# Performance work log

Hardware: AMD Instinct MI355X
Metric: run time of the kernel (lower is better)

## Reference

```python
import jax, jax.numpy as jnp
import numpy as np

KS = 3          # deformable kernel size
PAD = 1         # zero padding
N = KS * KS     # sampling points per pixel
INC = 64
OUTC = 64


def _conv(x, w, stride, pad, groups):
    return jax.lax.conv_general_dilated(
        x, w, (stride, stride), ((pad, pad), (pad, pad)),
        feature_group_count=groups,
        dimension_numbers=('NCHW', 'OIHW', 'NCHW'))


def setup_inputs() -> dict:
    key = jax.random.key(0)
    k = jax.random.split(key, 5)
    b, h, w = 4, 128, 128
    x = jax.random.normal(k[0], (b, INC, h, w), jnp.float32)
    # SeparableConv2d params (bias=False throughout in source)
    p_dw = jax.random.normal(k[1], (INC, 1, 3, 3), jnp.float32) * 0.1     # p_conv depthwise 3x3 pad1
    p_pw = jax.random.normal(k[2], (2 * N, INC, 1, 1), jnp.float32) * 0.1  # p_conv pointwise -> 2N offsets
    c_dw = jax.random.normal(k[3], (INC, 1, KS, KS), jnp.float32) * 0.1    # conv depthwise k=ks stride=ks
    c_pw = jax.random.normal(k[4], (OUTC, INC, 1, 1), jnp.float32) * 0.1   # conv pointwise
    return {'x': x, 'p_dw': p_dw, 'p_pw': p_pw, 'c_dw': c_dw, 'c_pw': c_pw}


def reference(x, p_dw, p_pw, c_dw, c_pw):
    b, c, h, w = x.shape
    offset = _conv(_conv(x, p_dw, 1, 1, INC), p_pw, 1, 0, 1)   # [b, 2N, h, w]
    xp = jnp.pad(x, ((0, 0), (0, 0), (PAD, PAD), (PAD, PAD)))  # zero_padding
    Hp, Wp = h + 2 * PAD, w + 2 * PAD
    # p_n: kernel-relative offsets (row-major over ks x ks, 'ij' meshgrid)
    r = jnp.arange(-(KS - 1) // 2, (KS - 1) // 2 + 1, dtype=jnp.float32)
    pnx, pny = jnp.meshgrid(r, r, indexing='ij')
    p_n = jnp.concatenate([pnx.ravel(), pny.ravel()])[None, :, None, None]  # [1, 2N, 1, 1]
    # p_0: base grid, 1-indexed (accounts for padding), stride=1
    gx = jnp.arange(1, h + 1, dtype=jnp.float32)[None, None, :, None]
    gy = jnp.arange(1, w + 1, dtype=jnp.float32)[None, None, None, :]
    p0 = jnp.concatenate([jnp.broadcast_to(gx, (1, N, h, w)),
                          jnp.broadcast_to(gy, (1, N, h, w))], axis=1)      # [1, 2N, h, w]
    p = (p0 + p_n + offset).transpose(0, 2, 3, 1)                           # [b, h, w, 2N]
    px, py = p[..., :N], p[..., N:]
    fx, fy = jnp.floor(px), jnp.floor(py)
    ltx = jnp.clip(fx, 0, Hp - 1); lty = jnp.clip(fy, 0, Wp - 1)
    rbx = jnp.clip(fx + 1, 0, Hp - 1); rby = jnp.clip(fy + 1, 0, Wp - 1)
    pxc = jnp.clip(px, 0, Hp - 1); pyc = jnp.clip(py, 0, Wp - 1)
    # bilinear weights
    g_lt = (1 + (ltx - pxc)) * (1 + (lty - pyc))
    g_rb = (1 - (rbx - pxc)) * (1 - (rby - pyc))
    g_lb = (1 + (ltx - pxc)) * (1 - (rby - pyc))
    g_rt = (1 - (rbx - pxc)) * (1 + (lty - pyc))
    x_flat = xp.reshape(b, c, Hp * Wp)

    def gather(qx, qy):  # -> [b, c, h, w, N]
        idx = (qx * Wp + qy).astype(jnp.int32).reshape(b, 1, h * w * N)
        return jnp.take_along_axis(x_flat, idx, axis=2).reshape(b, c, h, w, N)

    x_off = (g_lt[:, None] * gather(ltx, lty) + g_rb[:, None] * gather(rbx, rby)
             + g_lb[:, None] * gather(ltx, rby) + g_rt[:, None] * gather(rbx, lty))
    # _reshape_x_offset: [b,c,h,w,N] -> [b,c,h*ks,w*ks]
    x_off = x_off.reshape(b, c, h, w, KS, KS).transpose(0, 1, 2, 4, 3, 5).reshape(b, c, h * KS, w * KS)
    # SeparableConv2d(inc, outc, k=ks, stride=ks)
    return _conv(_conv(x_off, c_dw, KS, 0, INC), c_pw, 1, 0, 1)
```

## Files before the change

### kernel.cpp

```cpp
#include <hip/hip_runtime.h>
#include <hip/hip_fp16.h>

#define Hdim 128
#define Wdim 128
#define Cdim 64
#define HW   (Hdim * Wdim)
#define NPIX (4 * HW)
#define NBLK (NPIX / 64)
#define NXCD 8
#define Hp 130
#define HWp (Hp * Hp)

typedef _Float16 v8h __attribute__((ext_vector_type(8)));
typedef float    v4f __attribute__((ext_vector_type(4)));

__device__ __forceinline__ int xcd_swizzle(int bid, int nblk) {
    return (bid % NXCD) * (nblk / NXCD) + bid / NXCD;
}

__global__ __launch_bounds__(512) void transpose_kernel(
    const float* __restrict__ x,
    __half* __restrict__ xt)
{
    __shared__ float tile[64][65];
    int lane = threadIdx.x & 63;
    int g    = threadIdx.x >> 6;
    int blk  = xcd_swizzle(blockIdx.x, NBLK);
    int pix0 = blk * 64;
    int b    = pix0 >> 14;
    int hw0  = pix0 & (HW - 1);
    int h    = hw0 >> 7;
    int w0   = hw0 & 127;

    {
        int gid = blockIdx.x * 512 + threadIdx.x;
        if (gid < 2064 * 8) {
            int rp  = gid >> 3, sub = gid & 7;
            int img = rp / 516, pos = rp - img * 516;
            int i, j;
            if (pos < 130)      { i = 0;   j = pos; }
            else if (pos < 260) { i = 129; j = pos - 130; }
            else { int p2 = pos - 260; i = 1 + (p2 >> 1); j = (p2 & 1) ? 129 : 0; }
            float4* dst = (float4*)(xt + ((size_t)img * HWp + i * Hp + j) * Cdim);
            dst[sub] = make_float4(0.f, 0.f, 0.f, 0.f);
        }
    }

#pragma unroll
    for (int i = 0; i < 8; ++i) {
        int c = g * 8 + i;
        tile[c][lane] = x[(size_t)(b * Cdim + c) * HW + hw0 + lane];
    }
    __syncthreads();
#pragma unroll
    for (int i = 0; i < 8; ++i) {
        int p = g * 8 + i;
        size_t ppos = ((size_t)b * HWp + (h + 1) * Hp + (w0 + 1 + p)) * Cdim + lane;
        xt[ppos] = (__half)tile[lane][p];
    }
}

__global__ __launch_bounds__(512) void fused_kernel(
    const float* __restrict__ x,
    const float* __restrict__ p_dw,
    const float* __restrict__ p_pw,
    const __half* __restrict__ xt,
    const float* __restrict__ c_dw,
    const float* __restrict__ c_pw,
    float* __restrict__ out)
{
    __shared__ __align__(16) unsigned char smem[26880];
    __shared__ __align__(16) unsigned int geoL[8][320];

    auto part_h = (_Float16 (*)[18][64])smem;
    auto accs_h = (_Float16 (*)[72])smem;
    auto outD   = (float (*)[69])(smem + 9216);

    int lane = threadIdx.x & 63;
    int g    = threadIdx.x >> 6;
    int blk  = xcd_swizzle(blockIdx.x, NBLK);
    int pix0 = blk * 64;
    int pix  = pix0 + lane;
    int w = pix & (Wdim - 1);
    int h = (pix >> 7) & (Hdim - 1);
    int b = pix >> 14;

    int   off9[9];
    float msk9[9];
#pragma unroll
    for (int dh = -1; dh <= 1; ++dh) {
#pragma unroll
        for (int dw = -1; dw <= 1; ++dw) {
            int tap = (dh + 1) * 3 + (dw + 1);
            int hh = h + dh, ww = w + dw;
            bool ok = (hh >= 0) & (hh < Hdim) & (ww >= 0) & (ww < Wdim);
            off9[tap] = ok ? hh * Wdim + ww : 0;
            msk9[tap] = ok ? 1.f : 0.f;
        }
    }

    float t[8];
#pragma unroll
    for (int i = 0; i < 8; ++i) {
        int c = g * 8 + i;
        const float* xb0 = x + (size_t)(b * Cdim + c) * HW;
        float s = 0.f;
#pragma unroll
        for (int tap = 0; tap < 9; ++tap) {
            float v = xb0[off9[tap]] * msk9[tap];
            s += v * p_dw[c * 9 + tap];
        }
        t[i] = s;
    }

#pragma unroll
    for (int j = 0; j < 18; ++j) {
        float s = 0.f;
#pragma unroll
        for (int i = 0; i < 8; ++i)
            s += p_pw[j * Cdim + g * 8 + i] * t[i];
        part_h[g][j][lane] = (_Float16)s;
    }
    __syncthreads();

#pragma unroll
    for (int it = 0; it < 2; ++it) {
        int idx = threadIdx.x + it * 512;
        if (idx < 9 * 64) {
            int k = idx >> 6;
            int p = idx & 63;

            float offx = 0.f, offy = 0.f;
#pragma unroll
            for (int q = 0; q < 8; ++q) {
                offx += (float)part_h[q][k][p];
                offy += (float)part_h[q][k + 9][p];
            }

            int ppix = pix0 + p;
            int pw2 = ppix & (Wdim - 1);
            int ph2 = (ppix >> 7) & (Hdim - 1);

            float px = (float)(ph2 + 1) + (float)(k / 3 - 1) + offx;
            float py = (float)(pw2 + 1) + (float)(k % 3 - 1) + offy;

            float fx = floorf(px), fy = floorf(py);
            float ltx = fminf(fmaxf(fx, 0.f), 129.f);
            float lty = fminf(fmaxf(fy, 0.f), 129.f);
            float rbx = fminf(fmaxf(fx + 1.f, 0.f), 129.f);
            float rby = fminf(fmaxf(fy + 1.f, 0.f), 129.f);
            float pxc = fminf(fmaxf(px, 0.f), 129.f);
            float pyc = fminf(fmaxf(py, 0.f), 129.f);

            float glt = (1.f + ltx - pxc) * (1.f + lty - pyc);
            float grb = (1.f - rbx + pxc) * (1.f - rby + pyc);
            float glb = (1.f + ltx - pxc) * (1.f - rby + pyc);
            float grt = (1.f - rbx + pxc) * (1.f + lty - pyc);

            int ix0 = (int)ltx, iy0 = (int)lty, ix1 = (int)rbx, iy1 = (int)rby;

            unsigned int bb1, bb2;
            if (iy1 == iy0 + 1) {
                bb1 = (unsigned int)(ix0 * Hp + iy0) << 7;
                bb2 = (unsigned int)(ix1 * Hp + iy0) << 7;
            } else {
                glt = glb = grt = grb = 0.f;
                bb1 = bb2 = 0;
            }

            __half2 wlo = __floats2half2_rn(glt, grt);
            __half2 whi = __floats2half2_rn(glb, grb);
            uint4 pk;
            pk.x = *(const unsigned int*)&wlo;
            pk.y = *(const unsigned int*)&whi;
            pk.z = bb1;
            pk.w = bb2;
            *(uint4*)&geoL[p >> 3][(k * 8 + (p & 7)) * 4] = pk;
        }
    }
    __syncthreads();

    int c2   = lane & 31;
    bool lo  = lane < 32;
    int gu   = __builtin_amdgcn_readfirstlane(g);
    const char* xbB = (const char*)(xt + (size_t)b * HWp * Cdim) + (lane << 2);

    int gv0, gv1, gv2, gv3, gv4;
    {
        const unsigned int* gb = &geoL[gu][0] + lane;
        gv0 = gb[0];   gv1 = gb[64];  gv2 = gb[128];
        gv3 = gb[192]; gv4 = gb[256];
    }
    __half2 wk2h[9];
#pragma unroll
    for (int k = 0; k < 9; ++k)
        wk2h[k] = __floats2half2_rn(c_dw[(2 * c2) * 9 + k],
                                    c_dw[(2 * c2 + 1) * 9 + k]);

#define GV(r) ((r)==0?gv0:(r)==1?gv1:(r)==2?gv2:(r)==3?gv3:gv4)
#define RL(f) __builtin_amdgcn_readlane(GV((f) >> 6), (f) & 63)

    __half2 acch[8];
#pragma unroll
    for (int i = 0; i < 8; ++i) acch[i] = __floats2half2_rn(0.f, 0.f);

#pragma unroll
    for (int k = 0; k < 9; ++k) {
#pragma unroll
        for (int i = 0; i < 8; ++i) {
            const int f = (k * 8 + i) * 4;
            unsigned int d0 = (unsigned int)RL(f + 0);
            unsigned int d1 = (unsigned int)RL(f + 1);
            unsigned int bb1 = (unsigned int)RL(f + 2);
            unsigned int bb2 = (unsigned int)RL(f + 3);
            unsigned int v1 = *(const unsigned int*)(xbB + bb1);
            unsigned int v2 = *(const unsigned int*)(xbB + bb2);
            unsigned int wsu = lo ? d0 : d1;
            __half2 w12 = *(const __half2*)&wsu;
            __half2 v1h = *(const __half2*)&v1;
            __half2 v2h = *(const __half2*)&v2;
            __half2 tt = __hfma2(v2h, __half2half2(__high2half(w12)),
                                 __hmul2(v1h, __half2half2(__low2half(w12))));
            acch[i] = __hfma2(wk2h[k], tt, acch[i]);
        }
    }
#undef RL
#undef GV

#pragma unroll
    for (int i = 0; i < 8; ++i) {
        int me = *(int*)&acch[i];
        int ot = __shfl_xor(me, 32);
        acch[i] = __hadd2(acch[i], *(__half2*)&ot);
    }
    if (lo) {
#pragma unroll
        for (int i = 0; i < 8; ++i)
            *(__half2*)&accs_h[gu * 8 + i][2 * c2] = acch[i];
    }
    __syncthreads();

    {
        int pb = gu & 3;
        int ob = gu >> 2;
        int lr = lane & 15;
        int lg = lane >> 4;

        const v8h a0 = *(const v8h*)&accs_h[pb * 16 + lr][lg * 8];
        const v8h a1 = *(const v8h*)&accs_h[pb * 16 + lr][32 + lg * 8];

        v4f d0 = {0.f, 0.f, 0.f, 0.f}, d1 = {0.f, 0.f, 0.f, 0.f};
#pragma unroll
        for (int t2 = 0; t2 < 2; ++t2) {
            int oc = ob * 32 + t2 * 16 + lr;
            const float* wr = c_pw + oc * Cdim + lg * 8;
            v8h b0, b1;
#pragma unroll
            for (int j = 0; j < 8; ++j) {
                b0[j] = (_Float16)wr[j];
                b1[j] = (_Float16)wr[32 + j];
            }
            if (t2 == 0) {
                d0 = __builtin_amdgcn_mfma_f32_16x16x32_f16(a0, b0, d0, 0, 0, 0);
                d0 = __builtin_amdgcn_mfma_f32_16x16x32_f16(a1, b1, d0, 0, 0, 0);
            } else {
                d1 = __builtin_amdgcn_mfma_f32_16x16x32_f16(a0, b0, d1, 0, 0, 0);
                d1 = __builtin_amdgcn_mfma_f32_16x16x32_f16(a1, b1, d1, 0, 0, 0);
            }
        }

#pragma unroll
        for (int r = 0; r < 4; ++r) {
            outD[pb * 16 + lg * 4 + r][ob * 32 + lr]      = d0[r];
            outD[pb * 16 + lg * 4 + r][ob * 32 + 16 + lr] = d1[r];
        }
    }
    __syncthreads();

    int hw = pix & (HW - 1);
    size_t obase = (size_t)b * Cdim * HW + hw;
#pragma unroll
    for (int i = 0; i < 8; ++i)
        out[obase + (size_t)(gu * 8 + i) * HW] = outD[lane][gu * 8 + i];
}

extern "C" void kernel_launch(void* const* d_in, const int* in_sizes, int n_in,
                              void* d_out, int out_size, void* d_ws, size_t ws_size,
                              hipStream_t stream) {
    const float* x    = (const float*)d_in[0];
    const float* p_dw = (const float*)d_in[1];
    const float* p_pw = (const float*)d_in[2];
    const float* c_dw = (const float*)d_in[3];
    const float* c_pw = (const float*)d_in[4];
    float* out = (float*)d_out;

    __half* xt = (__half*)d_ws;

    transpose_kernel<<<dim3(NBLK), dim3(512), 0, stream>>>(x, xt);
    fused_kernel<<<dim3(NBLK), dim3(512), 0, stream>>>(x, p_dw, p_pw, xt, c_dw, c_pw, out);
}
```

Baseline: 50.88 us.

## Restructure deformable gather to 16-byte loads with lane-split corners and shuffle reduction

```diff
diff --git a/kernel.cpp b/kernel.cpp
--- a/kernel.cpp
+++ b/kernel.cpp
@@ -71,13 +71,15 @@
 {
     __shared__ __align__(16) unsigned char smem[26880];
     __shared__ __align__(16) unsigned int geoL[8][320];
+    __shared__ __align__(16) _Float16 cdw_h[9][64];
 
     auto part_h = (_Float16 (*)[18][64])smem;
     auto accs_h = (_Float16 (*)[72])smem;
     auto outD   = (float (*)[69])(smem + 9216);
 
-    int lane = threadIdx.x & 63;
-    int g    = threadIdx.x >> 6;
+    int tid  = threadIdx.x;
+    int lane = tid & 63;
+    int g    = tid >> 6;
     int blk  = xcd_swizzle(blockIdx.x, NBLK);
     int pix0 = blk * 64;
     int pix  = pix0 + lane;
@@ -121,11 +123,15 @@
             s += p_pw[j * Cdim + g * 8 + i] * t[i];
         part_h[g][j][lane] = (_Float16)s;
     }
+    for (int idx = tid; idx < 9 * 64; idx += 512) {
+        int k = idx >> 6, ch = idx & 63;
+        cdw_h[k][ch] = (_Float16)c_dw[ch * 9 + k];
+    }
     __syncthreads();
 
 #pragma unroll
     for (int it = 0; it < 2; ++it) {
-        int idx = threadIdx.x + it * 512;
+        int idx = tid + it * 512;
         if (idx < 9 * 64) {
             int k = idx >> 6;
             int p = idx & 63;
@@ -168,75 +174,81 @@
                 bb1 = bb2 = 0;
             }
 
-            __half2 wlo = __floats2half2_rn(glt, grt);
-            __half2 whi = __floats2half2_rn(glb, grb);
+            __half2 wr0 = __floats2half2_rn(glt, glb);
+            __half2 wr1 = __floats2half2_rn(grt, grb);
             uint4 pk;
-            pk.x = *(const unsigned int*)&wlo;
-            pk.y = *(const unsigned int*)&whi;
-            pk.z = bb1;
-            pk.w = bb2;
+            pk.x = bb1;
+            pk.y = bb2;
+            pk.z = *(const unsigned int*)&wr0;
+            pk.w = *(const unsigned int*)&wr1;
             *(uint4*)&geoL[p >> 3][(k * 8 + (p & 7)) * 4] = pk;
         }
     }
     __syncthreads();
 
-    int c2   = lane & 31;
-    bool lo  = lane < 32;
-    int gu   = __builtin_amdgcn_readfirstlane(g);
-    const char* xbB = (const char*)(xt + (size_t)b * HWp * Cdim) + (lane << 2);
-
-    int gv0, gv1, gv2, gv3, gv4;
-    {
-        const unsigned int* gb = &geoL[gu][0] + lane;
-        gv0 = gb[0];   gv1 = gb[64];  gv2 = gb[128];
-        gv3 = gb[192]; gv4 = gb[256];
-    }
-    __half2 wk2h[9];
-#pragma unroll
-    for (int k = 0; k < 9; ++k)
-        wk2h[k] = __floats2half2_rn(c_dw[(2 * c2) * 9 + k],
-                                    c_dw[(2 * c2 + 1) * 9 + k]);
-
-#define GV(r) ((r)==0?gv0:(r)==1?gv1:(r)==2?gv2:(r)==3?gv3:gv4)
-#define RL(f) __builtin_amdgcn_readlane(GV((f) >> 6), (f) & 63)
-
-    __half2 acch[8];
-#pragma unroll
-    for (int i = 0; i < 8; ++i) acch[i] = __floats2half2_rn(0.f, 0.f);
+    int gu  = __builtin_amdgcn_readfirstlane(g);
+    int pk_ = lane >> 5;
+    int sub = lane & 31;
+    int r_  = sub >> 4;
+    int s16 = sub & 15;
+    int cb  = s16 & 7;
+    int c_  = s16 >> 3;
+    int vsub = s16 * 16;
+
+    const char* geoB = (const char*)&geoL[0][0];
+    int addrB = gu * 1280 + pk_ * 16 + r_ * 4;
+    int addrW = addrB + 8 + c_ * 2;
+    const char* cdwB = (const char*)&cdw_h[0][0] + cb * 16;
+    const char* xbC  = (const char*)(xt + (size_t)b * HWp * Cdim);
+
+    __half2 acc[4][4];
+#pragma unroll
+    for (int q = 0; q < 4; ++q)
+#pragma unroll
+        for (int d = 0; d < 4; ++d) acc[q][d] = __floats2half2_rn(0.f, 0.f);
 
 #pragma unroll
     for (int k = 0; k < 9; ++k) {
-#pragma unroll
-        for (int i = 0; i < 8; ++i) {
-            const int f = (k * 8 + i) * 4;
-            unsigned int d0 = (unsigned int)RL(f + 0);
-            unsigned int d1 = (unsigned int)RL(f + 1);
-            unsigned int bb1 = (unsigned int)RL(f + 2);
-            unsigned int bb2 = (unsigned int)RL(f + 3);
-            unsigned int v1 = *(const unsigned int*)(xbB + bb1);
-            unsigned int v2 = *(const unsigned int*)(xbB + bb2);
-            unsigned int wsu = lo ? d0 : d1;
-            __half2 w12 = *(const __half2*)&wsu;
-            __half2 v1h = *(const __half2*)&v1;
-            __half2 v2h = *(const __half2*)&v2;
-            __half2 tt = __hfma2(v2h, __half2half2(__high2half(w12)),
-                                 __hmul2(v1h, __half2half2(__low2half(w12))));
-            acch[i] = __hfma2(wk2h[k], tt, acch[i]);
-        }
-    }
-#undef RL
-#undef GV
-
-#pragma unroll
-    for (int i = 0; i < 8; ++i) {
-        int me = *(int*)&acch[i];
-        int ot = __shfl_xor(me, 32);
-        acch[i] = __hadd2(acch[i], *(__half2*)&ot);
-    }
-    if (lo) {
-#pragma unroll
-        for (int i = 0; i < 8; ++i)
-            *(__half2*)&accs_h[gu * 8 + i][2 * c2] = acch[i];
+        const __half2* wkp = (const __half2*)(cdwB + k * 128);
+        __half2 wkA = wkp[0], wkB = wkp[1], wkC = wkp[2], wkD = wkp[3];
+#pragma unroll
+        for (int q = 0; q < 4; ++q) {
+            const int imm = (k * 8 + 2 * q) * 16;
+            unsigned int bb = *(const unsigned int*)(geoB + addrB + imm);
+            unsigned short wu = *(const unsigned short*)(geoB + addrW + imm);
+            uint4 v4 = *(const uint4*)(xbC + (bb + (unsigned int)vsub));
+            __half2 w2 = __half2half2(__ushort_as_half(wu));
+            const __half2* vv = (const __half2*)&v4;
+            acc[q][0] = __hfma2(wkA, __hmul2(w2, vv[0]), acc[q][0]);
+            acc[q][1] = __hfma2(wkB, __hmul2(w2, vv[1]), acc[q][1]);
+            acc[q][2] = __hfma2(wkC, __hmul2(w2, vv[2]), acc[q][2]);
+            acc[q][3] = __hfma2(wkD, __hmul2(w2, vv[3]), acc[q][3]);
+        }
+    }
+
+#pragma unroll
+    for (int q = 0; q < 4; ++q) {
+#pragma unroll
+        for (int d = 0; d < 4; ++d) {
+            int v = *(int*)&acc[q][d];
+            int o = __shfl_xor(v, 8);
+            __half2 tmp = __hadd2(acc[q][d], *(__half2*)&o);
+            int v2 = *(int*)&tmp;
+            int o2 = __shfl_xor(v2, 16);
+            acc[q][d] = __hadd2(tmp, *(__half2*)&o2);
+        }
+    }
+    if ((lane & 24) == 0) {
+#pragma unroll
+        for (int q = 0; q < 4; ++q) {
+            int i = 2 * q + pk_;
+            uint4 st;
+            st.x = *(unsigned int*)&acc[q][0];
+            st.y = *(unsigned int*)&acc[q][1];
+            st.z = *(unsigned int*)&acc[q][2];
+            st.w = *(unsigned int*)&acc[q][3];
+            *(uint4*)&accs_h[gu * 8 + i][cb * 8] = st;
+        }
     }
     __syncthreads();
 
```

Result: faster. 49.11 us, median of 3 (-3.5%).
